# Optimization experiments

Hardware: AMD Instinct MI355X
Metric: run time of the kernel (lower is better)

Reference implementation:

```python
import jax, jax.numpy as jnp
import numpy as np

HID = 64
IN_DIM = 38
NUM_LAYERS = 4
EPS = 1e-5
SLOPE = 0.01  # LeakyReLU default


def _leaky(x):
    return jnp.where(x >= 0, x, SLOPE * x)


def _batchnorm(x, g, b):
    # training-mode BatchNorm1d: batch statistics, biased variance
    m = jnp.mean(x, axis=0)
    v = jnp.mean((x - m) ** 2, axis=0)
    return (x - m) * jax.lax.rsqrt(v + EPS) * g + b


def _layernorm(x, g, b):
    m = jnp.mean(x, axis=-1, keepdims=True)
    v = jnp.mean((x - m) ** 2, axis=-1, keepdims=True)
    return (x - m) * jax.lax.rsqrt(v + EPS) * g + b


def setup_inputs() -> dict:
    key = jax.random.key(0)
    ks = jax.random.split(key, 12)
    N, E, NG = 100000, 1600000, 128
    edge_index = jax.random.randint(ks[0], (2, E), 0, N)
    n_feats = jax.random.normal(ks[1], (N, IN_DIM), dtype=jnp.float32)
    batch = jnp.sort(jax.random.randint(ks[2], (N,), 0, NG))

    def xavier(k, shape):
        fan_in, fan_out = shape[-2], shape[-1]
        lim = np.sqrt(6.0 / (fan_in + fan_out))
        return jax.random.uniform(k, shape, jnp.float32, -lim, lim)

    return {
        "edge_index": edge_index,
        "n_feats": n_feats,
        "batch": batch,
        "num_graphs": NG,
        "W_enc": xavier(ks[3], (IN_DIM, HID)),
        "b_enc": jnp.zeros((HID,), jnp.float32),
        "bn1_g": jnp.ones((HID,), jnp.float32),
        "bn1_b": jnp.zeros((HID,), jnp.float32),
        "a_w": xavier(ks[4], (NUM_LAYERS, 2 * HID, 1))[..., 0],  # [L, 2H]
        "lin_w": xavier(ks[5], (NUM_LAYERS, HID, HID)),
        "lin_b": jnp.zeros((NUM_LAYERS, HID), jnp.float32),
        "ln_g": jnp.ones((NUM_LAYERS, HID), jnp.float32),
        "ln_b": jnp.zeros((NUM_LAYERS, HID), jnp.float32),
        "bn2_g": jnp.ones((HID,), jnp.float32),
        "bn2_b": jnp.zeros((HID,), jnp.float32),
    }


def _update_v(feat, u, v, aw, lw, lb, lng, lnb):
    N = feat.shape[0]
    u_feat = feat[u]                      # [E, H] gather
    v_feat = feat[v]                      # [E, H] gather
    # attn = Linear([u||v]) with no bias -> split the weight
    attn = u_feat @ aw[:HID] + v_feat @ aw[HID:]      # [E]
    # segment softmax over edges grouped by destination v
    amax = jax.ops.segment_max(attn, v, num_segments=N)  # -inf for empty
    ex = jnp.exp(attn - amax[v])
    denom = jax.ops.segment_sum(ex, v, num_segments=N)
    w = ex / denom[v]                     # [E]
    msg = jax.ops.segment_sum(u_feat * w[:, None], v, num_segments=N)  # [N, H]
    return _leaky(_layernorm(msg @ lw + lb, lng, lnb))


def reference(edge_index, n_feats, batch, num_graphs, W_enc, b_enc, bn1_g, bn1_b,
              a_w, lin_w, lin_b, ln_g, ln_b, bn2_g, bn2_b):
    u, v = edge_index[0], edge_index[1]
    feat = _batchnorm(n_feats @ W_enc + b_enc, bn1_g, bn1_b)  # encoder
    acc = feat
    for l in range(NUM_LAYERS):
        feat = _update_v(feat, u, v, a_w[l], lin_w[l], lin_b[l], ln_g[l], ln_b[l])
        acc = acc + feat
    node_feats = acc / (NUM_LAYERS + 1)   # mean over layer outputs
    # scatter-mean over graphs
    sums = jax.ops.segment_sum(node_feats, batch, num_segments=num_graphs)
    cnts = jax.ops.segment_sum(jnp.ones_like(batch, jnp.float32), batch,
                               num_segments=num_graphs)
    prot = sums / jnp.maximum(cnts, 1.0)[:, None]
    return _leaky(_batchnorm(prot, bn2_g, bn2_b))
```

## Files before the change

### kernel.cpp

```cpp
#include <hip/hip_runtime.h>
#include <hip/hip_bf16.h>

#define HID 64
#define IN_DIM 38
#define NLAYERS 4
#define EPS 1e-5f
#define SLOPE 0.01f
#define ENC_ROWS 128
#define NBUK 256
#define CHUNK 4096

typedef __hip_bfloat16 bf16;
typedef unsigned int u32;
typedef __attribute__((ext_vector_type(8))) short short8;
typedef __attribute__((ext_vector_type(4))) float f32x4;

__device__ __forceinline__ float ldv(const float* p, int i) { return p[i]; }
__device__ __forceinline__ float ldv(const bf16* p, int i) { return __bfloat162float(p[i]); }

__device__ __forceinline__ short bfbits(float f) {
    bf16 h = __float2bfloat16(f);
    return *reinterpret_cast<short*>(&h);
}
__device__ __forceinline__ short ldbf(const bf16* p, int i) { return ((const short*)p)[i]; }
__device__ __forceinline__ short ldbf(const float* p, int i) { return bfbits(p[i]); }

__device__ __forceinline__ bool tag_is_bf16(const void* bn1g) {
    return *((const u32*)bn1g) != 0x3F800000u;
}

__device__ __forceinline__ float wred_sum(float v) {
    #pragma unroll
    for (int m = 32; m > 0; m >>= 1) v += __shfl_xor(v, m, 64);
    return v;
}

__device__ __forceinline__ float bflo(u32 w) { return __uint_as_float(w << 16); }
__device__ __forceinline__ float bfhi(u32 w) { return __uint_as_float(w & 0xFFFF0000u); }

__device__ __forceinline__ int bucket_of(int v, int N) {
    return (int)(((long long)v * NBUK) / N);
}

__global__ __launch_bounds__(256) void k_bcount(const int* __restrict__ ev, int E, int N,
                                                int* __restrict__ bcnt) {
    __shared__ int h[NBUK];
    h[threadIdx.x] = 0;
    __syncthreads();
    int base = blockIdx.x * CHUNK;
    int end = min(base + CHUNK, E);
    for (int i = base + threadIdx.x; i < end; i += 256) atomicAdd(&h[bucket_of(ev[i], N)], 1);
    __syncthreads();
    int c = h[threadIdx.x];
    if (c) atomicAdd(&bcnt[threadIdx.x], c);
}

__global__ void k_bscan(const int* __restrict__ bcnt, int* __restrict__ bbase,
                        int* __restrict__ bcur) {
    __shared__ int sm[NBUK];
    int t = threadIdx.x;
    int c = bcnt[t];
    sm[t] = c;
    __syncthreads();
    for (int ofs = 1; ofs < NBUK; ofs <<= 1) {
        int x = (t >= ofs) ? sm[t - ofs] : 0;
        __syncthreads();
        sm[t] += x;
        __syncthreads();
    }
    int excl = sm[t] - c;
    bbase[t] = excl;
    bcur[t] = excl;
    if (t == NBUK - 1) bbase[NBUK] = sm[t];
}

__global__ __launch_bounds__(256) void k_part(const int* __restrict__ eu,
                                              const int* __restrict__ ev, int E, int N,
                                              int* __restrict__ bcur, uint2* __restrict__ rec) {
    __shared__ int h[NBUK];
    int t = threadIdx.x;
    h[t] = 0;
    __syncthreads();
    int base = blockIdx.x * CHUNK;
    int end = min(base + CHUNK, E);
    for (int i = base + t; i < end; i += 256) atomicAdd(&h[bucket_of(ev[i], N)], 1);
    __syncthreads();
    int c = h[t];
    int rb = c ? atomicAdd(&bcur[t], c) : 0;
    __syncthreads();
    h[t] = rb;
    __syncthreads();
    for (int i = base + t; i < end; i += 256) {
        int u = eu[i], v = ev[i];
        int pos = atomicAdd(&h[bucket_of(v, N)], 1);
        rec[pos] = make_uint2((u32)u, (u32)v);
    }
}

__global__ __launch_bounds__(512) void k_csr(const uint2* __restrict__ rec,
                                             const int* __restrict__ bbase, int N, int E,
                                             int* __restrict__ row_ptr, int* __restrict__ col_u) {
    __shared__ int cnt[512], sc[512];
    int b = blockIdx.x;
    int t = threadIdx.x;
    int lo = (int)(((long long)b * N + NBUK - 1) / NBUK);
    int hi = (int)(((long long)(b + 1) * N + NBUK - 1) / NBUK);
    if (hi > N) hi = N;
    int nn = hi - lo;
    cnt[t] = 0;
    __syncthreads();
    int rlo = bbase[b], rhi = bbase[b + 1];
    for (int i = rlo + t; i < rhi; i += 512) atomicAdd(&cnt[(int)rec[i].y - lo], 1);
    __syncthreads();
    int c = cnt[t];
    sc[t] = c;
    __syncthreads();
    for (int ofs = 1; ofs < 512; ofs <<= 1) {
        int x = (t >= ofs) ? sc[t - ofs] : 0;
        __syncthreads();
        sc[t] += x;
        __syncthreads();
    }
    int excl = sc[t] - c;
    if (t < nn) row_ptr[lo + t] = rlo + excl;
    cnt[t] = rlo + excl;
    __syncthreads();
    for (int i = rlo + t; i < rhi; i += 512) {
        uint2 r = rec[i];
        int pos = atomicAdd(&cnt[(int)r.y - lo], 1);
        col_u[pos] = (int)r.x;
    }
    if (b == NBUK - 1 && t == 0) row_ptr[N] = E;
}

template <typename T>
__device__ __forceinline__ void encoder_body(const T* x, const T* W, const T* bias, int N,
                                             float* enc, float* bnsum, float* bnsq, float* sx) {
    int t = threadIdx.x;
    int lane = t & 63;
    int wid = t >> 6;
    int base = blockIdx.x * ENC_ROWS;
    int rows = min(ENC_ROWS, N - base);
    int total = rows * IN_DIM;
    for (int i = t; i < total; i += 256) sx[i] = ldv(x, base * IN_DIM + i);
    __syncthreads();

    float Wc[IN_DIM];
    #pragma unroll
    for (int k = 0; k < IN_DIM; k++) Wc[k] = ldv(W, k * 64 + lane);
    float bi = ldv(bias, lane);

    float s = 0.f, sq = 0.f;
    for (int r = wid * 32; r < wid * 32 + 32; r++) {
        int n = base + r;
        if (n >= N) break;
        float o = bi;
        #pragma unroll
        for (int k = 0; k < IN_DIM; k++) o += sx[r * IN_DIM + k] * Wc[k];
        enc[(size_t)n * 64 + lane] = o;
        s += o;
        sq += o * o;
    }
    __shared__ float ls[64], lq[64];
    if (t < 64) { ls[t] = 0.f; lq[t] = 0.f; }
    __syncthreads();
    atomicAdd(&ls[lane], s);
    atomicAdd(&lq[lane], sq);
    __syncthreads();
    if (t < 64) {
        atomicAdd(&bnsum[t], ls[t]);
        atomicAdd(&bnsq[t], lq[t]);
    }
}

__global__ __launch_bounds__(256) void k_encoder(const void* x, const void* W, const void* bias,
                                                 const void* tag, int N, float* enc, float* bnsum,
                                                 float* bnsq) {
    __shared__ float sx[ENC_ROWS * IN_DIM];
    if (tag_is_bf16(tag))
        encoder_body<bf16>((const bf16*)x, (const bf16*)W, (const bf16*)bias, N, enc, bnsum, bnsq,
                           sx);
    else
        encoder_body<float>((const float*)x, (const float*)W, (const float*)bias, N, enc, bnsum,
                            bnsq, sx);
}

__global__ void k_bn1fin(const float* __restrict__ bnsum, const float* __restrict__ bnsq, int N,
                         float* __restrict__ bn1m, float* __restrict__ bn1r) {
    int h = threadIdx.x;
    float m = bnsum[h] / (float)N;
    float v = bnsq[h] / (float)N - m * m;
    bn1m[h] = m;
    bn1r[h] = rsqrtf(v + EPS);
}

template <typename T>
__device__ __forceinline__ void bnapply_body(const float* enc, const float* bn1m,
                                             const float* bn1r, const T* g, const T* b,
                                             const T* aw0, int N, bf16* feat, float* exp_s) {
    int idx = blockIdx.x * 256 + threadIdx.x;
    int lane = threadIdx.x & 63;
    int n = idx >> 6;
    if (n >= N) return;
    float f = (enc[idx] - bn1m[lane]) * bn1r[lane] * ldv(g, lane) + ldv(b, lane);
    feat[idx] = __float2bfloat16(f);
    float s = wred_sum(f * ldv(aw0, lane));
    if (lane == 0) exp_s[n] = __expf(s);
}

__global__ __launch_bounds__(256) void k_bnapply(const float* enc, const float* bn1m,
                                                 const float* bn1r, const void* g, const void* b,
                                                 const void* aw0, const void* tag, int N,
                                                 bf16* feat, float* exp_s) {
    if (tag_is_bf16(tag))
        bnapply_body<bf16>(enc, bn1m, bn1r, (const bf16*)g, (const bf16*)b, (const bf16*)aw0, N,
                           feat, exp_s);
    else
        bnapply_body<float>(enc, bn1m, bn1r, (const float*)g, (const float*)b, (const float*)aw0,
                            N, feat, exp_s);
}

template <typename T>
__device__ __forceinline__ void layer_body(const int* __restrict__ row_ptr,
                                           const int* __restrict__ col_u,
                                           const float* __restrict__ exp_s,
                                           const bf16* __restrict__ feat, const T* lw, const T* lb,
                                           const T* lng, const T* lnb, const T* aw_next, int N,
                                           bf16* feat_out, float* exp_s_next,
                                           uint2 (*s_ue)[2][32], short* smsg, float (*ps)[4],
                                           float (*pq)[4], float (*pe)[4], float* mrs) {
    int lane = threadIdx.x & 63;
    int w = threadIdx.x >> 6;
    int half = lane >> 5;
    int h = lane & 31;
    int g = h >> 3;
    int cq = h & 7;
    int n0 = blockIdx.x * 16;

    #pragma unroll 1
    for (int it = 0; it < 2; it++) {
        int nl = w * 4 + it * 2 + half;
        int n = n0 + nl;
        int st = 0, en = 0;
        if (n < N) { st = row_ptr[n]; en = row_ptr[n + 1]; }
        float macc[8];
        #pragma unroll
        for (int x = 0; x < 8; x++) macc[x] = 0.f;
        float den = 0.f;

        for (int j0 = st; j0 < en; j0 += 32) {
            int jj = j0 + h;
            u32 uu = 0;
            float ee = 0.f;
            if (jj < en) {
                uu = (u32)col_u[jj];
                ee = exp_s[uu];
            }
            den += ee;
            s_ue[w][half][h] = make_uint2(uu, __float_as_uint(ee));
            int cnt = en - j0;
            if (cnt > 32) cnt = 32;
            int ng4 = (cnt + 3) >> 2;
            uint4 fv[8];
            float e4[8];
            #pragma unroll
            for (int k = 0; k < 8; k++) {
                if (k < ng4) {
                    uint2 ue = s_ue[w][half][k * 4 + g];
                    e4[k] = __uint_as_float(ue.y);
                    fv[k] = *(const uint4*)(feat + ((size_t)ue.x << 6) + (cq << 3));
                }
            }
            #pragma unroll
            for (int k = 0; k < 8; k++) {
                if (k < ng4) {
                    float e = e4[k];
                    macc[0] += e * bflo(fv[k].x);
                    macc[1] += e * bfhi(fv[k].x);
                    macc[2] += e * bflo(fv[k].y);
                    macc[3] += e * bfhi(fv[k].y);
                    macc[4] += e * bflo(fv[k].z);
                    macc[5] += e * bfhi(fv[k].z);
                    macc[6] += e * bflo(fv[k].w);
                    macc[7] += e * bfhi(fv[k].w);
                }
            }
        }

        #pragma unroll
        for (int m = 8; m <= 16; m <<= 1) {
            #pragma unroll
            for (int x = 0; x < 8; x++) macc[x] += __shfl_xor(macc[x], m, 64);
        }
        #pragma unroll
        for (int m = 1; m <= 16; m <<= 1) den += __shfl_xor(den, m, 64);
        float inv = (den > 0.f) ? 1.f / den : 0.f;
        if (g == 0) {
            short8 sv;
            #pragma unroll
            for (int x = 0; x < 8; x++) sv[x] = bfbits(macc[x] * inv);
            *(short8*)(smsg + nl * 72 + cq * 8) = sv;
        }
    }
    __syncthreads();

    int l15 = lane & 15;
    int q = lane >> 4;
    int col = w * 16 + l15;

    short8 bf0, bf1;
    #pragma unroll
    for (int j = 0; j < 8; j++) {
        bf0[j] = ldbf(lw, (q * 8 + j) * 64 + col);
        bf1[j] = ldbf(lw, (32 + q * 8 + j) * 64 + col);
    }
    short8 af0 = *(const short8*)(smsg + l15 * 72 + q * 8);
    short8 af1 = *(const short8*)(smsg + l15 * 72 + 32 + q * 8);
    float lbv = ldv(lb, col);
    f32x4 c = {lbv, lbv, lbv, lbv};
    c = __builtin_amdgcn_mfma_f32_16x16x32_bf16(af0, bf0, c, 0, 0, 0);
    c = __builtin_amdgcn_mfma_f32_16x16x32_bf16(af1, bf1, c, 0, 0, 0);

    float o[4], s1[4], s2[4];
    #pragma unroll
    for (int r = 0; r < 4; r++) {
        o[r] = c[r];
        s1[r] = o[r];
        s2[r] = o[r] * o[r];
    }
    #pragma unroll
    for (int m = 1; m <= 8; m <<= 1) {
        #pragma unroll
        for (int r = 0; r < 4; r++) {
            s1[r] += __shfl_xor(s1[r], m, 64);
            s2[r] += __shfl_xor(s2[r], m, 64);
        }
    }
    if (l15 == 0) {
        #pragma unroll
        for (int r = 0; r < 4; r++) {
            ps[q * 4 + r][w] = s1[r];
            pq[q * 4 + r][w] = s2[r];
        }
    }
    __syncthreads();
    if (threadIdx.x < 16) {
        int t = threadIdx.x;
        float S = ps[t][0] + ps[t][1] + ps[t][2] + ps[t][3];
        float Q = pq[t][0] + pq[t][1] + pq[t][2] + pq[t][3];
        float m = S * (1.f / 64.f);
        float var = Q * (1.f / 64.f) - m * m;
        mrs[t] = m;
        mrs[16 + t] = rsqrtf(var + EPS);
    }
    __syncthreads();

    float gcol = ldv(lng, col), bcol = ldv(lnb, col), awv = ldv(aw_next, col);
    float pexp[4];
    #pragma unroll
    for (int r = 0; r < 4; r++) {
        int row = q * 4 + r;
        int n = n0 + row;
        float y = (o[r] - mrs[row]) * mrs[16 + row] * gcol + bcol;
        y = (y >= 0.f) ? y : SLOPE * y;
        if (n < N) feat_out[n * 64 + col] = __float2bfloat16(y);
        pexp[r] = y * awv;
    }
    #pragma unroll
    for (int m = 1; m <= 8; m <<= 1) {
        #pragma unroll
        for (int r = 0; r < 4; r++) pexp[r] += __shfl_xor(pexp[r], m, 64);
    }
    if (l15 == 0) {
        #pragma unroll
        for (int r = 0; r < 4; r++) pe[q * 4 + r][w] = pexp[r];
    }
    __syncthreads();
    if (threadIdx.x < 16) {
        int t = threadIdx.x;
        int n = n0 + t;
        if (n < N) exp_s_next[n] = __expf(pe[t][0] + pe[t][1] + pe[t][2] + pe[t][3]);
    }
}

__global__ __launch_bounds__(256) void k_layer_off(const int* row_ptr, const int* col_u,
                                                   const float* exp_s, const bf16* feat,
                                                   const void* lw, const void* lb, const void* lng,
                                                   const void* lnb, const void* aw, const void* tag,
                                                   int lw_e, int v_e, int aw_e, int N,
                                                   bf16* feat_out, float* exp_s_next) {
    __shared__ uint2 s_ue[4][2][32];
    __shared__ short smsg[16 * 72];
    __shared__ float ps[16][4], pq[16][4], pe[16][4], mrs[32];
    if (tag_is_bf16(tag))
        layer_body<bf16>(row_ptr, col_u, exp_s, feat, (const bf16*)lw + lw_e, (const bf16*)lb + v_e,
                         (const bf16*)lng + v_e, (const bf16*)lnb + v_e, (const bf16*)aw + aw_e, N,
                         feat_out, exp_s_next, s_ue, smsg, ps, pq, pe, mrs);
    else
        layer_body<float>(row_ptr, col_u, exp_s, feat, (const float*)lw + lw_e,
                          (const float*)lb + v_e, (const float*)lng + v_e, (const float*)lnb + v_e,
                          (const float*)aw + aw_e, N, feat_out, exp_s_next, s_ue, smsg, ps, pq, pe,
                          mrs);
}

__global__ __launch_bounds__(256) void k_pool(const bf16* __restrict__ f0,
                                              const bf16* __restrict__ f1,
                                              const bf16* __restrict__ f2,
                                              const bf16* __restrict__ f3,
                                              const bf16* __restrict__ f4,
                                              const int* __restrict__ batch, int N,
                                              float* __restrict__ gsum, float* __restrict__ gcnt) {
    int lane = threadIdx.x & 63;
    int wave = blockIdx.x * 4 + (threadIdx.x >> 6);
    int n0 = wave * 64;
    if (n0 >= N) return;
    int nend = min(n0 + 64, N);
    float run = 0.f, cnt = 0.f;
    int cur = batch[n0];
    for (int n = n0; n < nend; n++) {
        int g = batch[n];
        int idx = n * 64 + lane;
        float v = (__bfloat162float(f0[idx]) + __bfloat162float(f1[idx]) +
                   __bfloat162float(f2[idx]) + __bfloat162float(f3[idx]) +
                   __bfloat162float(f4[idx])) *
                  (1.0f / (NLAYERS + 1));
        if (g != cur) {
            atomicAdd(&gsum[cur * 64 + lane], run);
            if (lane == 0) atomicAdd(&gcnt[cur], cnt);
            run = 0.f;
            cnt = 0.f;
            cur = g;
        }
        run += v;
        cnt += 1.f;
    }
    atomicAdd(&gsum[cur * 64 + lane], run);
    if (lane == 0) atomicAdd(&gcnt[cur], cnt);
}

template <typename T>
__device__ __forceinline__ void final_body(const float* gsum, const float* gcnt, int NG,
                                           const T* g2, const T* b2, T* out, float (*ps)[64],
                                           float (*pq)[64], float* stats) {
    int t = threadIdx.x;
    int h = t & 63;
    int p = t >> 6;
    float s = 0.f, q = 0.f;
    #pragma unroll 4
    for (int i = p; i < NG; i += 4) {
        float c = fmaxf(gcnt[i], 1.f);
        float v = gsum[i * 64 + h] / c;
        s += v;
        q += v * v;
    }
    ps[p][h] = s;
    pq[p][h] = q;
    __syncthreads();
    if (t < 64) {
        float S = ps[0][t] + ps[1][t] + ps[2][t] + ps[3][t];
        float Q = pq[0][t] + pq[1][t] + pq[2][t] + pq[3][t];
        float m = S / (float)NG;
        float var = Q / (float)NG - m * m;
        stats[t] = m;
        stats[64 + t] = rsqrtf(var + EPS);
    }
    __syncthreads();
    float m = stats[h];
    float r = stats[64 + h];
    float gg = ldv(g2, h), bb = ldv(b2, h);
    for (int i = p; i < NG; i += 4) {
        float c = fmaxf(gcnt[i], 1.f);
        float v = gsum[i * 64 + h] / c;
        float y = (v - m) * r * gg + bb;
        y = (y >= 0.f) ? y : SLOPE * y;
        out[i * 64 + h] = (T)y;
    }
}

__global__ __launch_bounds__(256) void k_final(const float* gsum, const float* gcnt, int NG,
                                               const void* g2, const void* b2, const void* tag,
                                               void* out) {
    __shared__ float ps[4][64], pq[4][64], stats[128];
    if (tag_is_bf16(tag))
        final_body<bf16>(gsum, gcnt, NG, (const bf16*)g2, (const bf16*)b2, (bf16*)out, ps, pq,
                         stats);
    else
        final_body<float>(gsum, gcnt, NG, (const float*)g2, (const float*)b2, (float*)out, ps, pq,
                          stats);
}

extern "C" void kernel_launch(void* const* d_in, const int* in_sizes, int n_in, void* d_out,
                              int out_size, void* d_ws, size_t ws_size, hipStream_t stream) {
    const int* edge_index = (const int*)d_in[0];
    const void* n_feats = d_in[1];
    const int* batch = (const int*)d_in[2];
    const void* W_enc = d_in[4];
    const void* b_enc = d_in[5];
    const void* bn1_g = d_in[6];
    const void* bn1_b = d_in[7];
    const void* a_w = d_in[8];
    const void* lin_w = d_in[9];
    const void* lin_b = d_in[10];
    const void* ln_g = d_in[11];
    const void* ln_b = d_in[12];
    const void* bn2_g = d_in[13];
    const void* bn2_b = d_in[14];

    const int E = in_sizes[0] / 2;
    const int N = in_sizes[1] / IN_DIM;
    const int NG = out_size / HID;
    const int* eu = edge_index;
    const int* ev = edge_index + E;

    char* base = (char*)d_ws;
    size_t off = 0;
    auto alloc = [&](size_t bytes) -> void* {
        void* p = base + off;
        off = (off + bytes + 255) & ~(size_t)255;
        return p;
    };
    int* bcnt = (int*)alloc(NBUK * 4);
    float* gsum = (float*)alloc((size_t)NG * 64 * 4);
    float* gcnt = (float*)alloc((size_t)NG * 4);
    float* bnsum = (float*)alloc(64 * 4);
    float* bnsq = (float*)alloc(64 * 4);
    size_t zbytes = off;
    int* bbase = (int*)alloc((NBUK + 1) * 4);
    int* bcur = (int*)alloc(NBUK * 4);
    int* row_ptr = (int*)alloc((size_t)(N + 1) * 4);
    int* col_u = (int*)alloc((size_t)E * 4);
    bf16* featbase = (bf16*)alloc((size_t)N * 64 * 2 * 5);
    float* eA = (float*)alloc((size_t)N * 4);
    float* eB = (float*)alloc((size_t)N * 4);
    float* bn1m = (float*)alloc(64 * 4);
    float* bn1r = (float*)alloc(64 * 4);
    (void)ws_size;

    bf16* feats[5];
    for (int l = 0; l < 5; l++) feats[l] = featbase + (size_t)l * N * 64;
    uint2* rec = (uint2*)feats[0];
    float* enc = (float*)feats[3];

    hipMemsetAsync(d_ws, 0, zbytes, stream);

    const int pb = (E + CHUNK - 1) / CHUNK;
    k_bcount<<<pb, 256, 0, stream>>>(ev, E, N, bcnt);
    k_bscan<<<1, NBUK, 0, stream>>>(bcnt, bbase, bcur);
    k_part<<<pb, 256, 0, stream>>>(eu, ev, E, N, bcur, rec);
    k_csr<<<NBUK, 512, 0, stream>>>(rec, bbase, N, E, row_ptr, col_u);

    k_encoder<<<(N + ENC_ROWS - 1) / ENC_ROWS, 256, 0, stream>>>(n_feats, W_enc, b_enc, bn1_g, N,
                                                                 enc, bnsum, bnsq);
    k_bn1fin<<<1, 64, 0, stream>>>(bnsum, bnsq, N, bn1m, bn1r);
    k_bnapply<<<(N * 64 + 255) / 256, 256, 0, stream>>>(enc, bn1m, bn1r, bn1_g, bn1_b, a_w, bn1_g,
                                                        N, feats[0], eA);

    float* ein = eA;
    float* eout = eB;
    for (int l = 0; l < NLAYERS; l++) {
        int lnext = (l + 1) & 3;
        k_layer_off<<<(N + 15) / 16, 256, 0, stream>>>(row_ptr, col_u, ein, feats[l], lin_w, lin_b,
                                                       ln_g, ln_b, a_w, bn1_g,
                                                        l * HID * HID,
                                                        l * HID,
                                                        lnext * 2 * HID, N, feats[l + 1],
                                                       eout);
        float* te = ein; ein = eout; eout = te;
    }

    int pw = (N + 63) / 64;
    k_pool<<<(pw + 3) / 4, 256, 0, stream>>>(feats[0], feats[1], feats[2], feats[3], feats[4],
                                             batch, N, gsum, gcnt);
    k_final<<<1, 256, 0, stream>>>(gsum, gcnt, NG, bn2_g, bn2_b, bn1_g, d_out);
}
```

Before: 446.1 us.

## Merge preprocessing kernels pairwise and reorder edge gather loads in layer kernel

```diff
diff --git a/kernel.cpp b/kernel.cpp
--- a/kernel.cpp
+++ b/kernel.cpp
@@ -42,58 +42,152 @@
     return (int)(((long long)v * NBUK) / N);
 }
 
-__global__ __launch_bounds__(256) void k_bcount(const int* __restrict__ ev, int E, int N,
-                                                int* __restrict__ bcnt) {
+template <typename T>
+__device__ __forceinline__ void encoder_body(int blk, const T* x, const T* W, const T* bias,
+                                             int N, float* enc, float* bnsum, float* bnsq,
+                                             float* sx, float* ls, float* lq) {
+    int t = threadIdx.x;
+    int lane = t & 63;
+    int wid = t >> 6;
+    int base = blk * ENC_ROWS;
+    int rows = min(ENC_ROWS, N - base);
+    int total = rows * IN_DIM;
+    for (int i = t; i < total; i += 256) sx[i] = ldv(x, base * IN_DIM + i);
+    __syncthreads();
+
+    float Wc[IN_DIM];
+    #pragma unroll
+    for (int k = 0; k < IN_DIM; k++) Wc[k] = ldv(W, k * 64 + lane);
+    float bi = ldv(bias, lane);
+
+    float s = 0.f, sq = 0.f;
+    for (int r = wid * 32; r < wid * 32 + 32; r++) {
+        int n = base + r;
+        if (n >= N) break;
+        float o = bi;
+        #pragma unroll
+        for (int k = 0; k < IN_DIM; k++) o += sx[r * IN_DIM + k] * Wc[k];
+        enc[(size_t)n * 64 + lane] = o;
+        s += o;
+        sq += o * o;
+    }
+    if (t < 64) { ls[t] = 0.f; lq[t] = 0.f; }
+    __syncthreads();
+    atomicAdd(&ls[lane], s);
+    atomicAdd(&lq[lane], sq);
+    __syncthreads();
+    if (t < 64) {
+        atomicAdd(&bnsum[t], ls[t]);
+        atomicAdd(&bnsq[t], lq[t]);
+    }
+}
+
+__global__ __launch_bounds__(256) void k_pre1(const int* __restrict__ ev, int E, int N,
+                                              int* __restrict__ bcnt, const void* x, const void* W,
+                                              const void* bias, const void* tag, float* enc,
+                                              float* bnsum, float* bnsq, int pb) {
+    __shared__ float sx[ENC_ROWS * IN_DIM];
+    __shared__ float ls[64], lq[64];
+    if ((int)blockIdx.x < pb) {
+        int* h = (int*)sx;
+        h[threadIdx.x] = 0;
+        __syncthreads();
+        int base = blockIdx.x * CHUNK;
+        int end = min(base + CHUNK, E);
+        for (int i = base + threadIdx.x; i < end; i += 256) atomicAdd(&h[bucket_of(ev[i], N)], 1);
+        __syncthreads();
+        int c = h[threadIdx.x];
+        if (c) atomicAdd(&bcnt[threadIdx.x], c);
+    } else {
+        int blk = blockIdx.x - pb;
+        if (tag_is_bf16(tag))
+            encoder_body<bf16>(blk, (const bf16*)x, (const bf16*)W, (const bf16*)bias, N, enc,
+                               bnsum, bnsq, sx, ls, lq);
+        else
+            encoder_body<float>(blk, (const float*)x, (const float*)W, (const float*)bias, N, enc,
+                                bnsum, bnsq, sx, ls, lq);
+    }
+}
+
+__global__ __launch_bounds__(256) void k_pre2(const int* __restrict__ bcnt, int* __restrict__ bbase,
+                                              int* __restrict__ bcur, const float* __restrict__ bnsum,
+                                              const float* __restrict__ bnsq, int N,
+                                              float* __restrict__ bn1m, float* __restrict__ bn1r) {
+    __shared__ int sm[NBUK];
+    if (blockIdx.x == 0) {
+        int t = threadIdx.x;
+        int c = bcnt[t];
+        sm[t] = c;
+        __syncthreads();
+        for (int ofs = 1; ofs < NBUK; ofs <<= 1) {
+            int x = (t >= ofs) ? sm[t - ofs] : 0;
+            __syncthreads();
+            sm[t] += x;
+            __syncthreads();
+        }
+        int excl = sm[t] - c;
+        bbase[t] = excl;
+        bcur[t] = excl;
+        if (t == NBUK - 1) bbase[NBUK] = sm[t];
+    } else {
+        int h = threadIdx.x;
+        if (h < 64) {
+            float m = bnsum[h] / (float)N;
+            float v = bnsq[h] / (float)N - m * m;
+            bn1m[h] = m;
+            bn1r[h] = rsqrtf(v + EPS);
+        }
+    }
+}
+
+template <typename T>
+__device__ __forceinline__ void bnapply_body(int blk, const float* enc, const float* bn1m,
+                                             const float* bn1r, const T* g, const T* b,
+                                             const T* aw0, int N, bf16* feat, float* exp_s) {
+    int idx = blk * 256 + threadIdx.x;
+    int lane = threadIdx.x & 63;
+    int n = idx >> 6;
+    if (n >= N) return;
+    float f = (enc[idx] - bn1m[lane]) * bn1r[lane] * ldv(g, lane) + ldv(b, lane);
+    feat[idx] = __float2bfloat16(f);
+    float s = wred_sum(f * ldv(aw0, lane));
+    if (lane == 0) exp_s[n] = __expf(s);
+}
+
+__global__ __launch_bounds__(256) void k_pre3(const int* __restrict__ eu,
+                                              const int* __restrict__ ev, int E, int N,
+                                              int* __restrict__ bcur, uint2* __restrict__ rec,
+                                              const float* enc, const float* bn1m,
+                                              const float* bn1r, const void* g, const void* b,
+                                              const void* aw0, const void* tag, bf16* feat0,
+                                              float* exp_s, int pb) {
     __shared__ int h[NBUK];
-    h[threadIdx.x] = 0;
-    __syncthreads();
-    int base = blockIdx.x * CHUNK;
-    int end = min(base + CHUNK, E);
-    for (int i = base + threadIdx.x; i < end; i += 256) atomicAdd(&h[bucket_of(ev[i], N)], 1);
-    __syncthreads();
-    int c = h[threadIdx.x];
-    if (c) atomicAdd(&bcnt[threadIdx.x], c);
-}
-
-__global__ void k_bscan(const int* __restrict__ bcnt, int* __restrict__ bbase,
-                        int* __restrict__ bcur) {
-    __shared__ int sm[NBUK];
-    int t = threadIdx.x;
-    int c = bcnt[t];
-    sm[t] = c;
-    __syncthreads();
-    for (int ofs = 1; ofs < NBUK; ofs <<= 1) {
-        int x = (t >= ofs) ? sm[t - ofs] : 0;
-        __syncthreads();
-        sm[t] += x;
-        __syncthreads();
-    }
-    int excl = sm[t] - c;
-    bbase[t] = excl;
-    bcur[t] = excl;
-    if (t == NBUK - 1) bbase[NBUK] = sm[t];
-}
-
-__global__ __launch_bounds__(256) void k_part(const int* __restrict__ eu,
-                                              const int* __restrict__ ev, int E, int N,
-                                              int* __restrict__ bcur, uint2* __restrict__ rec) {
-    __shared__ int h[NBUK];
-    int t = threadIdx.x;
-    h[t] = 0;
-    __syncthreads();
-    int base = blockIdx.x * CHUNK;
-    int end = min(base + CHUNK, E);
-    for (int i = base + t; i < end; i += 256) atomicAdd(&h[bucket_of(ev[i], N)], 1);
-    __syncthreads();
-    int c = h[t];
-    int rb = c ? atomicAdd(&bcur[t], c) : 0;
-    __syncthreads();
-    h[t] = rb;
-    __syncthreads();
-    for (int i = base + t; i < end; i += 256) {
-        int u = eu[i], v = ev[i];
-        int pos = atomicAdd(&h[bucket_of(v, N)], 1);
-        rec[pos] = make_uint2((u32)u, (u32)v);
+    if ((int)blockIdx.x < pb) {
+        int t = threadIdx.x;
+        h[t] = 0;
+        __syncthreads();
+        int base = blockIdx.x * CHUNK;
+        int end = min(base + CHUNK, E);
+        for (int i = base + t; i < end; i += 256) atomicAdd(&h[bucket_of(ev[i], N)], 1);
+        __syncthreads();
+        int c = h[t];
+        int rb = c ? atomicAdd(&bcur[t], c) : 0;
+        __syncthreads();
+        h[t] = rb;
+        __syncthreads();
+        for (int i = base + t; i < end; i += 256) {
+            int u = eu[i], v = ev[i];
+            int pos = atomicAdd(&h[bucket_of(v, N)], 1);
+            rec[pos] = make_uint2((u32)u, (u32)v);
+        }
+    } else {
+        int blk = blockIdx.x - pb;
+        if (tag_is_bf16(tag))
+            bnapply_body<bf16>(blk, enc, bn1m, bn1r, (const bf16*)g, (const bf16*)b,
+                               (const bf16*)aw0, N, feat0, exp_s);
+        else
+            bnapply_body<float>(blk, enc, bn1m, bn1r, (const float*)g, (const float*)b,
+                                (const float*)aw0, N, feat0, exp_s);
     }
 }
 
@@ -134,100 +228,13 @@
 }
 
 template <typename T>
-__device__ __forceinline__ void encoder_body(const T* x, const T* W, const T* bias, int N,
-                                             float* enc, float* bnsum, float* bnsq, float* sx) {
-    int t = threadIdx.x;
-    int lane = t & 63;
-    int wid = t >> 6;
-    int base = blockIdx.x * ENC_ROWS;
-    int rows = min(ENC_ROWS, N - base);
-    int total = rows * IN_DIM;
-    for (int i = t; i < total; i += 256) sx[i] = ldv(x, base * IN_DIM + i);
-    __syncthreads();
-
-    float Wc[IN_DIM];
-    #pragma unroll
-    for (int k = 0; k < IN_DIM; k++) Wc[k] = ldv(W, k * 64 + lane);
-    float bi = ldv(bias, lane);
-
-    float s = 0.f, sq = 0.f;
-    for (int r = wid * 32; r < wid * 32 + 32; r++) {
-        int n = base + r;
-        if (n >= N) break;
-        float o = bi;
-        #pragma unroll
-        for (int k = 0; k < IN_DIM; k++) o += sx[r * IN_DIM + k] * Wc[k];
-        enc[(size_t)n * 64 + lane] = o;
-        s += o;
-        sq += o * o;
-    }
-    __shared__ float ls[64], lq[64];
-    if (t < 64) { ls[t] = 0.f; lq[t] = 0.f; }
-    __syncthreads();
-    atomicAdd(&ls[lane], s);
-    atomicAdd(&lq[lane], sq);
-    __syncthreads();
-    if (t < 64) {
-        atomicAdd(&bnsum[t], ls[t]);
-        atomicAdd(&bnsq[t], lq[t]);
-    }
-}
-
-__global__ __launch_bounds__(256) void k_encoder(const void* x, const void* W, const void* bias,
-                                                 const void* tag, int N, float* enc, float* bnsum,
-                                                 float* bnsq) {
-    __shared__ float sx[ENC_ROWS * IN_DIM];
-    if (tag_is_bf16(tag))
-        encoder_body<bf16>((const bf16*)x, (const bf16*)W, (const bf16*)bias, N, enc, bnsum, bnsq,
-                           sx);
-    else
-        encoder_body<float>((const float*)x, (const float*)W, (const float*)bias, N, enc, bnsum,
-                            bnsq, sx);
-}
-
-__global__ void k_bn1fin(const float* __restrict__ bnsum, const float* __restrict__ bnsq, int N,
-                         float* __restrict__ bn1m, float* __restrict__ bn1r) {
-    int h = threadIdx.x;
-    float m = bnsum[h] / (float)N;
-    float v = bnsq[h] / (float)N - m * m;
-    bn1m[h] = m;
-    bn1r[h] = rsqrtf(v + EPS);
-}
-
-template <typename T>
-__device__ __forceinline__ void bnapply_body(const float* enc, const float* bn1m,
-                                             const float* bn1r, const T* g, const T* b,
-                                             const T* aw0, int N, bf16* feat, float* exp_s) {
-    int idx = blockIdx.x * 256 + threadIdx.x;
-    int lane = threadIdx.x & 63;
-    int n = idx >> 6;
-    if (n >= N) return;
-    float f = (enc[idx] - bn1m[lane]) * bn1r[lane] * ldv(g, lane) + ldv(b, lane);
-    feat[idx] = __float2bfloat16(f);
-    float s = wred_sum(f * ldv(aw0, lane));
-    if (lane == 0) exp_s[n] = __expf(s);
-}
-
-__global__ __launch_bounds__(256) void k_bnapply(const float* enc, const float* bn1m,
-                                                 const float* bn1r, const void* g, const void* b,
-                                                 const void* aw0, const void* tag, int N,
-                                                 bf16* feat, float* exp_s) {
-    if (tag_is_bf16(tag))
-        bnapply_body<bf16>(enc, bn1m, bn1r, (const bf16*)g, (const bf16*)b, (const bf16*)aw0, N,
-                           feat, exp_s);
-    else
-        bnapply_body<float>(enc, bn1m, bn1r, (const float*)g, (const float*)b, (const float*)aw0,
-                            N, feat, exp_s);
-}
-
-template <typename T>
 __device__ __forceinline__ void layer_body(const int* __restrict__ row_ptr,
                                            const int* __restrict__ col_u,
                                            const float* __restrict__ exp_s,
                                            const bf16* __restrict__ feat, const T* lw, const T* lb,
                                            const T* lng, const T* lnb, const T* aw_next, int N,
-                                           bf16* feat_out, float* exp_s_next,
-                                           uint2 (*s_ue)[2][32], short* smsg, float (*ps)[4],
+                                           bf16* feat_out, float* exp_s_next, u32 (*s_u)[2][32],
+                                           float (*s_e)[2][32], short* smsg, float (*ps)[4],
                                            float (*pq)[4], float (*pe)[4], float* mrs) {
     int lane = threadIdx.x & 63;
     int w = threadIdx.x >> 6;
@@ -250,26 +257,32 @@
 
         for (int j0 = st; j0 < en; j0 += 32) {
             int jj = j0 + h;
+            bool valid = jj < en;
             u32 uu = 0;
-            float ee = 0.f;
-            if (jj < en) {
-                uu = (u32)col_u[jj];
-                ee = exp_s[uu];
-            }
-            den += ee;
-            s_ue[w][half][h] = make_uint2(uu, __float_as_uint(ee));
+            if (valid) uu = (u32)col_u[jj];
+            s_u[w][half][h] = uu;
             int cnt = en - j0;
             if (cnt > 32) cnt = 32;
             int ng4 = (cnt + 3) >> 2;
+
+            float ee = 0.f;
+            if (valid) ee = exp_s[uu];
+            u32 su[8];
             uint4 fv[8];
+            #pragma unroll
+            for (int k = 0; k < 8; k++) {
+                if (k < ng4) su[k] = s_u[w][half][k * 4 + g];
+            }
+            #pragma unroll
+            for (int k = 0; k < 8; k++) {
+                if (k < ng4) fv[k] = *(const uint4*)(feat + ((size_t)su[k] << 6) + (cq << 3));
+            }
+            den += ee;
+            s_e[w][half][h] = ee;
             float e4[8];
             #pragma unroll
             for (int k = 0; k < 8; k++) {
-                if (k < ng4) {
-                    uint2 ue = s_ue[w][half][k * 4 + g];
-                    e4[k] = __uint_as_float(ue.y);
-                    fv[k] = *(const uint4*)(feat + ((size_t)ue.x << 6) + (cq << 3));
-                }
+                if (k < ng4) e4[k] = s_e[w][half][k * 4 + g];
             }
             #pragma unroll
             for (int k = 0; k < 8; k++) {
@@ -389,18 +402,19 @@
                                                    const void* lnb, const void* aw, const void* tag,
                                                    int lw_e, int v_e, int aw_e, int N,
                                                    bf16* feat_out, float* exp_s_next) {
-    __shared__ uint2 s_ue[4][2][32];
+    __shared__ u32 s_u[4][2][32];
+    __shared__ float s_e[4][2][32];
     __shared__ short smsg[16 * 72];
     __shared__ float ps[16][4], pq[16][4], pe[16][4], mrs[32];
     if (tag_is_bf16(tag))
         layer_body<bf16>(row_ptr, col_u, exp_s, feat, (const bf16*)lw + lw_e, (const bf16*)lb + v_e,
                          (const bf16*)lng + v_e, (const bf16*)lnb + v_e, (const bf16*)aw + aw_e, N,
-                         feat_out, exp_s_next, s_ue, smsg, ps, pq, pe, mrs);
+                         feat_out, exp_s_next, s_u, s_e, smsg, ps, pq, pe, mrs);
     else
         layer_body<float>(row_ptr, col_u, exp_s, feat, (const float*)lw + lw_e,
                           (const float*)lb + v_e, (const float*)lng + v_e, (const float*)lnb + v_e,
-                          (const float*)aw + aw_e, N, feat_out, exp_s_next, s_ue, smsg, ps, pq, pe,
-                          mrs);
+                          (const float*)aw + aw_e, N, feat_out, exp_s_next, s_u, s_e, smsg, ps, pq,
+                          pe, mrs);
 }
 
 __global__ __launch_bounds__(256) void k_pool(const bf16* __restrict__ f0,
@@ -529,6 +543,7 @@
     int* bcur = (int*)alloc(NBUK * 4);
     int* row_ptr = (int*)alloc((size_t)(N + 1) * 4);
     int* col_u = (int*)alloc((size_t)E * 4);
+    uint2* rec = (uint2*)alloc((size_t)E * 8);
     bf16* featbase = (bf16*)alloc((size_t)N * 64 * 2 * 5);
     float* eA = (float*)alloc((size_t)N * 4);
     float* eB = (float*)alloc((size_t)N * 4);
@@ -538,22 +553,20 @@
 
     bf16* feats[5];
     for (int l = 0; l < 5; l++) feats[l] = featbase + (size_t)l * N * 64;
-    uint2* rec = (uint2*)feats[0];
     float* enc = (float*)feats[3];
 
     hipMemsetAsync(d_ws, 0, zbytes, stream);
 
     const int pb = (E + CHUNK - 1) / CHUNK;
-    k_bcount<<<pb, 256, 0, stream>>>(ev, E, N, bcnt);
-    k_bscan<<<1, NBUK, 0, stream>>>(bcnt, bbase, bcur);
-    k_part<<<pb, 256, 0, stream>>>(eu, ev, E, N, bcur, rec);
+    const int encB = (N + ENC_ROWS - 1) / ENC_ROWS;
+    const int bnapB = (N * 64 + 255) / 256;
+
+    k_pre1<<<pb + encB, 256, 0, stream>>>(ev, E, N, bcnt, n_feats, W_enc, b_enc, bn1_g, enc,
+                                          bnsum, bnsq, pb);
+    k_pre2<<<2, 256, 0, stream>>>(bcnt, bbase, bcur, bnsum, bnsq, N, bn1m, bn1r);
+    k_pre3<<<pb + bnapB, 256, 0, stream>>>(eu, ev, E, N, bcur, rec, enc, bn1m, bn1r, bn1_g,
+                                           bn1_b, a_w, bn1_g, feats[0], eA, pb);
     k_csr<<<NBUK, 512, 0, stream>>>(rec, bbase, N, E, row_ptr, col_u);
-
-    k_encoder<<<(N + ENC_ROWS - 1) / ENC_ROWS, 256, 0, stream>>>(n_feats, W_enc, b_enc, bn1_g, N,
-                                                                 enc, bnsum, bnsq);
-    k_bn1fin<<<1, 64, 0, stream>>>(bnsum, bnsq, N, bn1m, bn1r);
-    k_bnapply<<<(N * 64 + 255) / 256, 256, 0, stream>>>(enc, bn1m, bn1r, bn1_g, bn1_b, a_w, bn1_g,
-                                                        N, feats[0], eA);
 
     float* ein = eA;
     float* eout = eB;
```

Measured after the change: 447.4 us. Within noise of the previous version (+0.3%).
